# Kernel optimization log

Hardware: AMD Instinct MI355X
Metric: run time of the kernel (lower is better)

The kernel has to match this reference:

```python
import jax, jax.numpy as jnp
import numpy as np

NUM_HEADS = 8
D_MODEL = 512
HEAD_DIM = D_MODEL // NUM_HEADS
LN_EPS = 1e-5


def setup_inputs() -> dict:
    key = jax.random.key(0)
    ks = jax.random.split(key, 12)
    B, S = 8, 1024
    P = 2 * S - 1  # relative position length
    s = 0.02
    return {
        "x": jax.random.normal(ks[0], (B, S, D_MODEL), jnp.float32),
        "pos_emb": jax.random.normal(ks[1], (P, D_MODEL), jnp.float32),
        "ln_w": jnp.ones((D_MODEL,), jnp.float32),
        "ln_b": jnp.zeros((D_MODEL,), jnp.float32),
        "Wq": jax.random.normal(ks[2], (D_MODEL, D_MODEL), jnp.float32) * s,
        "bq": jax.random.normal(ks[3], (D_MODEL,), jnp.float32) * s,
        "Wk": jax.random.normal(ks[4], (D_MODEL, D_MODEL), jnp.float32) * s,
        "bk": jax.random.normal(ks[5], (D_MODEL,), jnp.float32) * s,
        "Wv": jax.random.normal(ks[6], (D_MODEL, D_MODEL), jnp.float32) * s,
        "bv": jax.random.normal(ks[7], (D_MODEL,), jnp.float32) * s,
        "Wo": jax.random.normal(ks[8], (D_MODEL, D_MODEL), jnp.float32) * s,
        "bo": jax.random.normal(ks[9], (D_MODEL,), jnp.float32) * s,
        "Wp": jax.random.normal(ks[10], (D_MODEL, D_MODEL), jnp.float32) * s,
        "pos_bias_u": jax.random.normal(ks[11], (D_MODEL,), jnp.float32) * s,
        "pos_bias_v": jax.random.normal(jax.random.fold_in(key, 99), (D_MODEL,), jnp.float32) * s,
    }


def _rel_shift(x):
    # x: [B, H, S, P] -> Transformer-XL relative shift, return [B, H, S, S]
    b, h, s, p = x.shape
    x = jnp.pad(x, ((0, 0), (0, 0), (0, 0), (1, 0)))  # pad one zero column on left
    x = x.reshape(b, h, p + 1, s)[:, :, 1:, :]
    x = x.reshape(b, h, s, p)
    return x[:, :, :, :s]


def reference(x, pos_emb, ln_w, ln_b, Wq, bq, Wk, bk, Wv, bv, Wo, bo, Wp,
              pos_bias_u, pos_bias_v):
    B, S, D = x.shape
    H, hd = NUM_HEADS, HEAD_DIM
    # LayerNorm
    mu = jnp.mean(x, axis=-1, keepdims=True)
    var = jnp.mean(jnp.square(x - mu), axis=-1, keepdims=True)
    h_ = (x - mu) * jax.lax.rsqrt(var + LN_EPS) * ln_w + ln_b
    # Projections (torch Linear: y = x @ W.T + b)
    q = (h_ @ Wq.T + bq).reshape(B, S, H, hd).transpose(0, 2, 1, 3)  # [B,H,S,hd]
    k = (h_ @ Wk.T + bk).reshape(B, S, H, hd).transpose(0, 2, 1, 3)
    v = (h_ @ Wv.T + bv).reshape(B, S, H, hd).transpose(0, 2, 1, 3)
    bias_u = pos_bias_u.reshape(1, H, 1, hd)
    bias_v = pos_bias_v.reshape(1, H, 1, hd)
    content = jnp.einsum('bhqd,bhkd->bhqk', q + bias_u, k)
    # Positional projection: [P, D] -> [H, P, hd]
    p = (pos_emb @ Wp.T).reshape(-1, H, hd).transpose(1, 0, 2)
    pos_score = jnp.einsum('bhqd,hpd->bhqp', q + bias_v, p)
    pos_score = _rel_shift(pos_score)
    scale = 1.0 / np.sqrt(hd).astype(np.float32)
    attn = jax.nn.softmax((content + pos_score) * scale, axis=-1)
    out = jnp.einsum('bhqk,bhkd->bhqd', attn, v)
    out = out.transpose(0, 2, 1, 3).reshape(B, S, D)
    out = out @ Wo.T + bo
    return x + out
```

## Files before the change

kernel.cpp:

```cpp
#include <hip/hip_runtime.h>
#include <hip/hip_bf16.h>


typedef __attribute__((ext_vector_type(8))) short  s16x8;
typedef __attribute__((ext_vector_type(4))) short  s16x4;
typedef __attribute__((ext_vector_type(8))) __bf16 bfv8;
typedef __attribute__((ext_vector_type(4))) float  f32x4;

__device__ __forceinline__ float b2f(short s){
  unsigned u = ((unsigned)(unsigned short)s) << 16;
  float f; __builtin_memcpy(&f, &u, 4); return f;
}
__device__ __forceinline__ short f2b(float f){
  unsigned u; __builtin_memcpy(&u, &f, 4);
  u = (u + 0x7fffu + ((u >> 16) & 1u)) >> 16;
  return (short)u;
}
__device__ __forceinline__ f32x4 MFMA(s16x8 a, s16x8 b, f32x4 c){
  return __builtin_amdgcn_mfma_f32_16x16x32_bf16(
      __builtin_bit_cast(bfv8, a), __builtin_bit_cast(bfv8, b), c, 0, 0, 0);
}
__device__ __forceinline__ void gload_lds16(const void* g, void* l){
  __builtin_amdgcn_global_load_lds(
      (const __attribute__((address_space(1))) void*)g,
      (__attribute__((address_space(3))) void*)l, 16, 0, 0);
}
__device__ __forceinline__ void cvt8(const float* in, short* out, size_t i8){
  f32x4 a = *(const f32x4*)(in + i8*8);
  f32x4 b = *(const f32x4*)(in + i8*8 + 4);
  short o[8];
  o[0]=f2b(a[0]); o[1]=f2b(a[1]); o[2]=f2b(a[2]); o[3]=f2b(a[3]);
  o[4]=f2b(b[0]); o[5]=f2b(b[1]); o[6]=f2b(b[2]); o[7]=f2b(b[3]);
  *(s16x8*)(out + i8*8) = *(s16x8*)o;
}

__global__ __launch_bounds__(256) void prep_kernel(
    const float* __restrict__ Wq, const float* __restrict__ Wk,
    const float* __restrict__ Wv, const float* __restrict__ Wo,
    const float* __restrict__ Wp, const float* __restrict__ pos,
    const float* __restrict__ x, const float* __restrict__ lnw, const float* __restrict__ lnb,
    short* __restrict__ wqkv, short* __restrict__ wo, short* __restrict__ wp,
    short* __restrict__ posbf, short* __restrict__ h_bf)
{
  int bid = blockIdx.x, tid = threadIdx.x;
  if(bid < 640){
    int w = bid >> 7;
    size_t i = (size_t)(bid & 127)*256 + tid;
    const float* src; short* dst;
    if(w == 0){ src = Wq; dst = wqkv; }
    else if(w == 1){ src = Wk; dst = wqkv + 262144; }
    else if(w == 2){ src = Wv; dst = wqkv + 524288; }
    else if(w == 3){ src = Wo; dst = wo; }
    else { src = Wp; dst = wp; }
    cvt8(src, dst, i);
  } else if(bid < 1152){
    size_t i = (size_t)(bid - 640)*256 + tid;
    if(i < 131008) cvt8(pos, posbf, i);
  } else {
    int row = (bid - 1152)*4 + (tid >> 6);
    int lane = tid & 63;
    const float* xr = x + (size_t)row*512;
    f32x4 v0 = *(const f32x4*)(xr + lane*8);
    f32x4 v1 = *(const f32x4*)(xr + lane*8 + 4);
    float s  = v0[0]+v0[1]+v0[2]+v0[3]+v1[0]+v1[1]+v1[2]+v1[3];
    float s2 = v0[0]*v0[0]+v0[1]*v0[1]+v0[2]*v0[2]+v0[3]*v0[3]
             + v1[0]*v1[0]+v1[1]*v1[1]+v1[2]*v1[2]+v1[3]*v1[3];
    #pragma unroll
    for(int m=1;m<64;m<<=1){ s += __shfl_xor(s,m); s2 += __shfl_xor(s2,m); }
    float mu = s * (1.0f/512.0f);
    float rs = rsqrtf(s2*(1.0f/512.0f) - mu*mu + 1e-5f);
    short o[8];
    #pragma unroll
    for(int e=0;e<8;e++){
      float xv = (e<4)? v0[e] : v1[e-4];
      int d = lane*8 + e;
      o[e] = f2b((xv - mu)*rs*lnw[d] + lnb[d]);
    }
    *(s16x8*)(h_bf + (size_t)row*512 + lane*8) = *(s16x8*)o;
  }
}

__global__ __launch_bounds__(256) void gemm_fused(
    const short* __restrict__ h_bf, const short* __restrict__ wqkv,
    const float* __restrict__ bq, const float* __restrict__ bk, const float* __restrict__ bv,
    const short* __restrict__ posbf, const short* __restrict__ wp,
    short* __restrict__ q_sw, short* __restrict__ k_sw, short* __restrict__ v_sw,
    short* __restrict__ p_sw)
{
  __shared__ __align__(16) short At[128*32];
  __shared__ __align__(16) short Bt[128*32];
  int bid = blockIdx.x, tid = threadIdx.x;
  int wave = tid >> 6, lane = tid & 63;
  int quad = lane >> 4, l16 = lane & 15;
  int srow = lane >> 2, scol = (lane & 3)*8;
  if(bid < 768){
    int bx = bid % 12, by = bid / 12;
    int m0 = by*128, n0 = bx*128;
    int wm = wave >> 1, wn = wave & 1;
    f32x4 acc[4][4] = {};
    for(int k0=0; k0<512; k0+=32){
      #pragma unroll
      for(int c=0;c<2;c++){
        int rb = (wave + 4*c)*16;
        gload_lds16(h_bf + (size_t)(m0 + rb + srow)*512 + k0 + scol, At + rb*32);
        gload_lds16(wqkv + (size_t)(n0 + rb + srow)*512 + k0 + scol, Bt + rb*32);
      }
      __syncthreads();
      s16x8 af[4], bfr[4];
      #pragma unroll
      for(int i=0;i<4;i++) af[i]  = *(const s16x8*)(At + (wm*64 + i*16 + l16)*32 + quad*8);
      #pragma unroll
      for(int j=0;j<4;j++) bfr[j] = *(const s16x8*)(Bt + (wn*64 + j*16 + l16)*32 + quad*8);
      #pragma unroll
      for(int i=0;i<4;i++)
        #pragma unroll
        for(int j=0;j<4;j++)
          acc[i][j] = MFMA(af[i], bfr[j], acc[i][j]);
      __syncthreads();
    }
    #pragma unroll
    for(int i=0;i<4;i++){
      int rowb = m0 + wm*64 + i*16 + quad*4;
      #pragma unroll
      for(int j=0;j<4;j++){
        int colg = n0 + wn*64 + j*16 + l16;
        int seg = colg >> 9, c = colg & 511;
        float bias = (seg == 0) ? bq[c] : (seg == 1) ? bk[c] : bv[c];
        int hh = c >> 6;
        if(seg < 2){
          int ks = (c>>5)&1, qd = (c>>3)&3, e = c&7;
          int tblk = (rowb>>4)&63, bb = rowb>>10;
          short* dst = seg ? k_sw : q_sw;
          size_t base = ((size_t)((((bb*8+hh)*64+tblk)*2+ks)*64) + qd*16)*8 + e;
          #pragma unroll
          for(int r=0;r<4;r++)
            dst[base + (size_t)(quad*4+r)*8] = f2b(acc[i][j][r] + bias);
        } else {
          int ds = (c>>4)&3, l16p = c&15;
          int jt = (rowb>>6)&15, jk = (rowb>>5)&1, qd = (rowb>>3)&3, e0 = rowb&7;
          int bb = rowb>>10;
          short o4[4];
          #pragma unroll
          for(int r=0;r<4;r++) o4[r] = f2b(acc[i][j][r] + bias);
          size_t base = ((size_t)(((((bb*8+hh)*16+jt)*4+ds)*2+jk)*64) + qd*16 + l16p)*8 + e0;
          *(s16x4*)(v_sw + base) = *(s16x4*)o4;
        }
      }
    }
  } else {
    int pid = bid - 768;
    int bx = pid % 8, by = pid / 8;
    int m0 = by*64, n0 = bx*64;
    int wm = wave >> 1, wn = wave & 1;
    f32x4 acc[2][2] = {};
    for(int k0=0; k0<512; k0+=32){
      int rb = wave*16;
      int ra = m0 + rb + srow; if(ra > 2046) ra = 2046;
      gload_lds16(posbf + (size_t)ra*512 + k0 + scol, At + rb*32);
      gload_lds16(wp + (size_t)(n0 + rb + srow)*512 + k0 + scol, Bt + rb*32);
      __syncthreads();
      s16x8 af[2], bfr[2];
      #pragma unroll
      for(int i=0;i<2;i++) af[i]  = *(const s16x8*)(At + (wm*32 + i*16 + l16)*32 + quad*8);
      #pragma unroll
      for(int j=0;j<2;j++) bfr[j] = *(const s16x8*)(Bt + (wn*32 + j*16 + l16)*32 + quad*8);
      #pragma unroll
      for(int i=0;i<2;i++)
        #pragma unroll
        for(int j=0;j<2;j++)
          acc[i][j] = MFMA(af[i], bfr[j], acc[i][j]);
      __syncthreads();
    }
    #pragma unroll
    for(int i=0;i<2;i++){
      int rowb = m0 + wm*32 + i*16 + quad*4;
      #pragma unroll
      for(int j=0;j<2;j++){
        int col = n0 + wn*32 + j*16 + l16;
        int hh = col>>6, ks = (col>>5)&1, qd = (col>>3)&3, e = col&7;
        int rblk = rowb>>4;
        size_t base = ((size_t)(((hh*128+rblk)*2+ks)*64) + qd*16)*8 + e;
        #pragma unroll
        for(int r=0;r<4;r++)
          p_sw[base + (size_t)(quad*4+r)*8] = f2b(acc[i][j][r]);
      }
    }
  }
}

__global__ __launch_bounds__(256) void attn_kernel(
    const short* __restrict__ q_sw, const short* __restrict__ k_sw,
    const short* __restrict__ v_sw, const short* __restrict__ p_sw,
    const float* __restrict__ bu, const float* __restrict__ bvv,
    short* __restrict__ out)
{
  __shared__ __align__(16) float combf[4160];
  int tid = threadIdx.x;
  int wave = tid >> 6, lane = tid & 63, quad = lane >> 4, l16 = lane & 15;
  int h = blockIdx.y, b = blockIdx.z, bh = b*8 + h;
  int iblk = blockIdx.x;
  int iw = iblk*16;
  short* pw = (short*)combf + wave*1152;

  const short* qb = q_sw + (size_t)bh*65536;
  const short* kb = k_sw + (size_t)bh*65536;
  const short* vb = v_sw + (size_t)bh*65536;
  const short* pb = p_sw + (size_t)h*131072;

  s16x8 qu[2], qv[2];
  #pragma unroll
  for(int ks=0;ks<2;ks++){
    s16x8 qr = *(const s16x8*)(qb + ((size_t)(iblk*2+ks)*64 + lane)*8);
    short tu[8], tv[8];
    #pragma unroll
    for(int e=0;e<8;e++){
      int d = h*64 + ks*32 + quad*8 + e;
      float f = b2f(qr[e]);
      tu[e] = f2b((f + bu[d]) * 0.125f);
      tv[e] = f2b((f + bvv[d]) * 0.125f);
    }
    qu[ks] = *(s16x8*)tu; qv[ks] = *(s16x8*)tv;
  }

  f32x4 oacc[4] = {};
  float lpart[4] = {0.f, 0.f, 0.f, 0.f};

  #pragma unroll
  for(int t=0; t<4; t++){
    int jt = wave*4 + t;
    f32x4 sc[4];
    #pragma unroll
    for(int js=0;js<4;js++){
      f32x4 a = {};
      #pragma unroll
      for(int ks=0;ks<2;ks++){
        s16x8 kf = *(const s16x8*)(kb + ((size_t)((jt*4+js)*2+ks)*64 + lane)*8);
        a = MFMA(qu[ks], kf, a);
      }
      sc[js] = a;
    }
    int rb0 = (jt*64 - iw + 1008) >> 4;
    f32x4 ps[5];
    #pragma unroll
    for(int nt=0;nt<5;nt++){
      f32x4 a = {};
      #pragma unroll
      for(int ks=0;ks<2;ks++){
        s16x8 pf = *(const s16x8*)(pb + ((size_t)((rb0+nt)*2+ks)*64 + lane)*8);
        a = MFMA(qv[ks], pf, a);
      }
      ps[nt] = a;
    }
    #pragma unroll
    for(int r=0;r<4;r++){
      int il = quad*4 + r;
      int srcl = quad*16 + ((l16 + 15 - il) & 15);
      float rot[5];
      #pragma unroll
      for(int nt=0;nt<5;nt++) rot[nt] = __shfl(ps[nt][r], srcl);
      bool lo = (l16 <= il);
      #pragma unroll
      for(int js=0;js<4;js++){
        float sv = sc[js][r] + (lo ? rot[js] : rot[js+1]);
        float pe = __expf(sv);
        lpart[r] += pe;
        pw[il*72 + js*16 + l16] = f2b(pe);
      }
    }
    #pragma unroll
    for(int jk=0;jk<2;jk++){
      s16x8 pf = *(const s16x8*)(pw + l16*72 + jk*32 + quad*8);
      #pragma unroll
      for(int ds=0;ds<4;ds++){
        s16x8 vf = *(const s16x8*)(vb + ((size_t)((jt*4+ds)*2+jk)*64 + lane)*8);
        oacc[ds] = MFMA(pf, vf, oacc[ds]);
      }
    }
  }
  #pragma unroll
  for(int r=0;r<4;r++){
    float l = lpart[r];
    #pragma unroll
    for(int m=1;m<16;m<<=1) l += __shfl_xor(l, m);
    lpart[r] = l;
  }
  __syncthreads();
  float* comb  = combf;
  float* lcomb = combf + 4096;
  #pragma unroll
  for(int e=0;e<16;e++) comb[wave*1024 + e*64 + lane] = oacc[e>>2][e&3];
  if(l16 == 0){
    #pragma unroll
    for(int r=0;r<4;r++) lcomb[wave*16 + quad*4 + r] = lpart[r];
  }
  __syncthreads();
  #pragma unroll
  for(int i=0;i<4;i++){
    int s = i*256 + tid;
    int e = s >> 6, lsrc = s & 63;
    int ds = e >> 2, rr = e & 3;
    int il = (lsrc >> 4)*4 + rr;
    int dim = ds*16 + (lsrc & 15);
    float o = comb[s] + comb[1024+s] + comb[2048+s] + comb[3072+s];
    float l = lcomb[il] + lcomb[16+il] + lcomb[32+il] + lcomb[48+il];
    out[((size_t)(b*1024 + iw + il)*512) + h*64 + dim] = f2b(o / l);
  }
}

__global__ __launch_bounds__(256) void gemm_out(
    const short* __restrict__ A, const short* __restrict__ B,
    const float* __restrict__ bias, const float* __restrict__ resid,
    float* __restrict__ Cout)
{
  __shared__ __align__(16) short At[64*32];
  __shared__ __align__(16) short Bt[64*32];
  int tid = threadIdx.x;
  int wave = tid >> 6, lane = tid & 63;
  int quad = lane >> 4, l16 = lane & 15;
  int wm = wave >> 1, wn = wave & 1;
  int m0 = blockIdx.y*64, n0 = blockIdx.x*64;
  int srow = lane >> 2, scol = (lane & 3)*8;
  f32x4 acc[2][2] = {};
  for(int k0=0; k0<512; k0+=32){
    int rb = wave*16;
    gload_lds16(A + (size_t)(m0 + rb + srow)*512 + k0 + scol, At + rb*32);
    gload_lds16(B + (size_t)(n0 + rb + srow)*512 + k0 + scol, Bt + rb*32);
    __syncthreads();
    s16x8 af[2], bfr[2];
    #pragma unroll
    for(int i=0;i<2;i++) af[i]  = *(const s16x8*)(At + (wm*32 + i*16 + l16)*32 + quad*8);
    #pragma unroll
    for(int j=0;j<2;j++) bfr[j] = *(const s16x8*)(Bt + (wn*32 + j*16 + l16)*32 + quad*8);
    #pragma unroll
    for(int i=0;i<2;i++)
      #pragma unroll
      for(int j=0;j<2;j++)
        acc[i][j] = MFMA(af[i], bfr[j], acc[i][j]);
    __syncthreads();
  }
  #pragma unroll
  for(int i=0;i<2;i++){
    int rowb = m0 + wm*32 + i*16 + quad*4;
    #pragma unroll
    for(int j=0;j<2;j++){
      int col = n0 + wn*32 + j*16 + l16;
      float bv = bias[col];
      #pragma unroll
      for(int r=0;r<4;r++){
        size_t idx = (size_t)(rowb + r)*512 + col;
        Cout[idx] = acc[i][j][r] + bv + resid[idx];
      }
    }
  }
}

extern "C" void kernel_launch(void* const* d_in, const int* in_sizes, int n_in,
                              void* d_out, int out_size, void* d_ws, size_t ws_size,
                              hipStream_t stream)
{
  const float* x    = (const float*)d_in[0];
  const float* pos  = (const float*)d_in[1];
  const float* lnw  = (const float*)d_in[2];
  const float* lnb  = (const float*)d_in[3];
  const float* Wq   = (const float*)d_in[4];
  const float* bq   = (const float*)d_in[5];
  const float* Wk   = (const float*)d_in[6];
  const float* bk   = (const float*)d_in[7];
  const float* Wv   = (const float*)d_in[8];
  const float* bv   = (const float*)d_in[9];
  const float* Wo   = (const float*)d_in[10];
  const float* bo   = (const float*)d_in[11];
  const float* Wp   = (const float*)d_in[12];
  const float* pbu  = (const float*)d_in[13];
  const float* pbv  = (const float*)d_in[14];
  float* out = (float*)d_out;

  char* ws = (char*)d_ws;
  short* h_bf    = (short*)(ws);
  short* q_sw    = (short*)(ws + ( 8u<<20));
  short* k_sw    = (short*)(ws + (16u<<20));
  short* v_sw    = (short*)(ws + (24u<<20));
  short* a_bf    = (short*)(ws + (32u<<20));
  short* p_sw    = (short*)(ws + (40u<<20));
  short* pos_bf  = (short*)(ws + (42u<<20));
  short* wqkv_bf = (short*)(ws + (44u<<20));
  short* wo_bf   = (short*)(ws + (47u<<20));
  short* wp_bf   = (short*)(ws + (47u<<20) + (512u<<10));

  prep_kernel<<<dim3(3200), 256, 0, stream>>>(Wq, Wk, Wv, Wo, Wp, pos,
                                              x, lnw, lnb,
                                              wqkv_bf, wo_bf, wp_bf, pos_bf, h_bf);
  gemm_fused<<<dim3(1024), 256, 0, stream>>>(h_bf, wqkv_bf, bq, bk, bv,
                                             pos_bf, wp_bf,
                                             q_sw, k_sw, v_sw, p_sw);
  attn_kernel<<<dim3(64,8,8), 256, 0, stream>>>(q_sw, k_sw, v_sw, p_sw, pbu, pbv, a_bf);
  gemm_out<<<dim3(8,128), 256, 0, stream>>>(a_bf, wo_bf, bo, x, out);
  (void)in_sizes; (void)n_in; (void)out_size; (void)ws_size;
}
```

Measured before the change: 233.3 us.

## Stage QKV epilogue through LDS, use packed bf16 converts and exp2 softmax

```diff
diff --git a/kernel.cpp b/kernel.cpp
--- a/kernel.cpp
+++ b/kernel.cpp
@@ -3,7 +3,6 @@
 
 
 typedef __attribute__((ext_vector_type(8))) short  s16x8;
-typedef __attribute__((ext_vector_type(4))) short  s16x4;
 typedef __attribute__((ext_vector_type(8))) __bf16 bfv8;
 typedef __attribute__((ext_vector_type(4))) float  f32x4;
 
@@ -16,6 +15,10 @@
   u = (u + 0x7fffu + ((u >> 16) & 1u)) >> 16;
   return (short)u;
 }
+__device__ __forceinline__ unsigned pk2(float lo, float hi){
+  __hip_bfloat162 t = __float22bfloat162_rn(make_float2(lo, hi));
+  unsigned u; __builtin_memcpy(&u, &t, 4); return u;
+}
 __device__ __forceinline__ f32x4 MFMA(s16x8 a, s16x8 b, f32x4 c){
   return __builtin_amdgcn_mfma_f32_16x16x32_bf16(
       __builtin_bit_cast(bfv8, a), __builtin_bit_cast(bfv8, b), c, 0, 0, 0);
@@ -25,13 +28,14 @@
       (const __attribute__((address_space(1))) void*)g,
       (__attribute__((address_space(3))) void*)l, 16, 0, 0);
 }
+typedef __attribute__((ext_vector_type(4))) unsigned u32x4;
 __device__ __forceinline__ void cvt8(const float* in, short* out, size_t i8){
   f32x4 a = *(const f32x4*)(in + i8*8);
   f32x4 b = *(const f32x4*)(in + i8*8 + 4);
-  short o[8];
-  o[0]=f2b(a[0]); o[1]=f2b(a[1]); o[2]=f2b(a[2]); o[3]=f2b(a[3]);
-  o[4]=f2b(b[0]); o[5]=f2b(b[1]); o[6]=f2b(b[2]); o[7]=f2b(b[3]);
-  *(s16x8*)(out + i8*8) = *(s16x8*)o;
+  u32x4 o;
+  o[0] = pk2(a[0],a[1]); o[1] = pk2(a[2],a[3]);
+  o[2] = pk2(b[0],b[1]); o[3] = pk2(b[2],b[3]);
+  *(u32x4*)(out + i8*8) = o;
 }
 
 __global__ __launch_bounds__(256) void prep_kernel(
@@ -69,14 +73,16 @@
     for(int m=1;m<64;m<<=1){ s += __shfl_xor(s,m); s2 += __shfl_xor(s2,m); }
     float mu = s * (1.0f/512.0f);
     float rs = rsqrtf(s2*(1.0f/512.0f) - mu*mu + 1e-5f);
-    short o[8];
+    float y[8];
     #pragma unroll
     for(int e=0;e<8;e++){
       float xv = (e<4)? v0[e] : v1[e-4];
       int d = lane*8 + e;
-      o[e] = f2b((xv - mu)*rs*lnw[d] + lnb[d]);
-    }
-    *(s16x8*)(h_bf + (size_t)row*512 + lane*8) = *(s16x8*)o;
+      y[e] = (xv - mu)*rs*lnw[d] + lnb[d];
+    }
+    u32x4 o;
+    o[0]=pk2(y[0],y[1]); o[1]=pk2(y[2],y[3]); o[2]=pk2(y[4],y[5]); o[3]=pk2(y[6],y[7]);
+    *(u32x4*)(h_bf + (size_t)row*512 + lane*8) = o;
   }
 }
 
@@ -87,8 +93,9 @@
     short* __restrict__ q_sw, short* __restrict__ k_sw, short* __restrict__ v_sw,
     short* __restrict__ p_sw)
 {
-  __shared__ __align__(16) short At[128*32];
-  __shared__ __align__(16) short Bt[128*32];
+  __shared__ __align__(16) short smem[9216];
+  short* At = smem;
+  short* Bt = smem + 4096;
   int bid = blockIdx.x, tid = threadIdx.x;
   int wave = tid >> 6, lane = tid & 63;
   int quad = lane >> 4, l16 = lane & 15;
@@ -118,33 +125,75 @@
           acc[i][j] = MFMA(af[i], bfr[j], acc[i][j]);
       __syncthreads();
     }
-    #pragma unroll
-    for(int i=0;i<4;i++){
-      int rowb = m0 + wm*64 + i*16 + quad*4;
-      #pragma unroll
-      for(int j=0;j<4;j++){
-        int colg = n0 + wn*64 + j*16 + l16;
-        int seg = colg >> 9, c = colg & 511;
-        float bias = (seg == 0) ? bq[c] : (seg == 1) ? bk[c] : bv[c];
-        int hh = c >> 6;
-        if(seg < 2){
-          int ks = (c>>5)&1, qd = (c>>3)&3, e = c&7;
-          int tblk = (rowb>>4)&63, bb = rowb>>10;
-          short* dst = seg ? k_sw : q_sw;
-          size_t base = ((size_t)((((bb*8+hh)*64+tblk)*2+ks)*64) + qd*16)*8 + e;
+    int seg = bx >> 2;
+    int nseg = (bx & 3)*128;
+    int bb = by >> 3;
+    const float* bsrc = (seg==0)? bq : (seg==1)? bk : bv;
+    float bias_j[4];
+    #pragma unroll
+    for(int j=0;j<4;j++) bias_j[j] = bsrc[nseg + wn*64 + j*16 + l16];
+    if(seg < 2){
+      short* dst = seg ? k_sw : q_sw;
+      #pragma unroll
+      for(int h2=0; h2<2; h2++){
+        if(wm == h2){
           #pragma unroll
-          for(int r=0;r<4;r++)
-            dst[base + (size_t)(quad*4+r)*8] = f2b(acc[i][j][r] + bias);
-        } else {
-          int ds = (c>>4)&3, l16p = c&15;
-          int jt = (rowb>>6)&15, jk = (rowb>>5)&1, qd = (rowb>>3)&3, e0 = rowb&7;
-          int bb = rowb>>10;
-          short o4[4];
+          for(int i=0;i<4;i++){
+            int lr = i*16 + quad*4;
+            #pragma unroll
+            for(int j=0;j<4;j++){
+              int cl = wn*64 + j*16 + l16;
+              unsigned p01 = pk2(acc[i][j][0]+bias_j[j], acc[i][j][1]+bias_j[j]);
+              unsigned p23 = pk2(acc[i][j][2]+bias_j[j], acc[i][j][3]+bias_j[j]);
+              smem[(lr+0)*136 + cl] = (short)p01;
+              smem[(lr+1)*136 + cl] = (short)(p01>>16);
+              smem[(lr+2)*136 + cl] = (short)p23;
+              smem[(lr+3)*136 + cl] = (short)(p23>>16);
+            }
+          }
+        }
+        __syncthreads();
+        #pragma unroll
+        for(int it=0; it<4; it++){
+          int ci = it*4 + wave;
+          int hs = ci >> 2, tb = ci & 3;
+          s16x8 vv = *(const s16x8*)(smem + (tb*16 + l16)*136 + hs*32 + quad*8);
+          int hh = (nseg>>6) + (hs>>1);
+          int tg = ((m0 + h2*64)>>4) + tb;
+          size_t chunk = ((size_t)((bb*8 + hh)*64 + tg))*2 + (hs&1);
+          *(s16x8*)(dst + chunk*512 + (size_t)lane*8) = vv;
+        }
+        __syncthreads();
+      }
+    } else {
+      #pragma unroll
+      for(int h2=0; h2<2; h2++){
+        int jt = by*2 + h2;
+        if(wm == h2){
           #pragma unroll
-          for(int r=0;r<4;r++) o4[r] = f2b(acc[i][j][r] + bias);
-          size_t base = ((size_t)(((((bb*8+hh)*16+jt)*4+ds)*2+jk)*64) + qd*16 + l16p)*8 + e0;
-          *(s16x4*)(v_sw + base) = *(s16x4*)o4;
+          for(int i=0;i<4;i++){
+            int tl = i*16 + quad*4;
+            #pragma unroll
+            for(int j=0;j<4;j++){
+              int dl = wn*64 + j*16 + l16;
+              unsigned p01 = pk2(acc[i][j][0]+bias_j[j], acc[i][j][1]+bias_j[j]);
+              unsigned p23 = pk2(acc[i][j][2]+bias_j[j], acc[i][j][3]+bias_j[j]);
+              unsigned* w2 = (unsigned*)(smem + dl*72 + tl);
+              w2[0] = p01; w2[1] = p23;
+            }
+          }
         }
+        __syncthreads();
+        #pragma unroll
+        for(int it=0; it<4; it++){
+          int ci = it*4 + wave;
+          int hl = ci>>3, ds = (ci>>1)&3, jk = ci&1;
+          s16x8 vv = *(const s16x8*)(smem + (hl*64 + ds*16 + l16)*72 + jk*32 + quad*8);
+          int hh = (nseg>>6) + hl;
+          size_t chunk = (((size_t)((bb*8 + hh)*16 + jt))*4 + ds)*2 + jk;
+          *(s16x8*)(v_sw + chunk*512 + (size_t)lane*8) = vv;
+        }
+        __syncthreads();
       }
     }
   } else {
@@ -207,6 +256,7 @@
   const short* vb = v_sw + (size_t)bh*65536;
   const short* pb = p_sw + (size_t)h*131072;
 
+  const float S2 = 0.125f * 1.44269504f;
   s16x8 qu[2], qv[2];
   #pragma unroll
   for(int ks=0;ks<2;ks++){
@@ -216,10 +266,18 @@
     for(int e=0;e<8;e++){
       int d = h*64 + ks*32 + quad*8 + e;
       float f = b2f(qr[e]);
-      tu[e] = f2b((f + bu[d]) * 0.125f);
-      tv[e] = f2b((f + bvv[d]) * 0.125f);
+      tu[e] = f2b((f + bu[d]) * S2);
+      tv[e] = f2b((f + bvv[d]) * S2);
     }
     qu[ks] = *(s16x8*)tu; qv[ks] = *(s16x8*)tv;
+  }
+
+  int srcl[4]; bool lo[4];
+  #pragma unroll
+  for(int r=0;r<4;r++){
+    int il = quad*4 + r;
+    srcl[r] = quad*16 + ((l16 + 15 - il) & 15);
+    lo[r]   = (l16 <= il);
   }
 
   f32x4 oacc[4] = {};
@@ -251,21 +309,29 @@
       }
       ps[nt] = a;
     }
+    float pe[4][4];
     #pragma unroll
     for(int r=0;r<4;r++){
-      int il = quad*4 + r;
-      int srcl = quad*16 + ((l16 + 15 - il) & 15);
       float rot[5];
       #pragma unroll
-      for(int nt=0;nt<5;nt++) rot[nt] = __shfl(ps[nt][r], srcl);
-      bool lo = (l16 <= il);
+      for(int nt=0;nt<5;nt++) rot[nt] = __shfl(ps[nt][r], srcl[r]);
       #pragma unroll
       for(int js=0;js<4;js++){
-        float sv = sc[js][r] + (lo ? rot[js] : rot[js+1]);
-        float pe = __expf(sv);
-        lpart[r] += pe;
-        pw[il*72 + js*16 + l16] = f2b(pe);
-      }
+        float sv = sc[js][r] + (lo[r] ? rot[js] : rot[js+1]);
+        float p = exp2f(sv);
+        pe[js][r] = p;
+        lpart[r] += p;
+      }
+    }
+    #pragma unroll
+    for(int js=0;js<4;js++){
+      int col = js*16 + l16;
+      unsigned p01 = pk2(pe[js][0], pe[js][1]);
+      unsigned p23 = pk2(pe[js][2], pe[js][3]);
+      pw[(quad*4+0)*72 + col] = (short)p01;
+      pw[(quad*4+1)*72 + col] = (short)(p01>>16);
+      pw[(quad*4+2)*72 + col] = (short)p23;
+      pw[(quad*4+3)*72 + col] = (short)(p23>>16);
     }
     #pragma unroll
     for(int jk=0;jk<2;jk++){
@@ -303,7 +369,8 @@
     int dim = ds*16 + (lsrc & 15);
     float o = comb[s] + comb[1024+s] + comb[2048+s] + comb[3072+s];
     float l = lcomb[il] + lcomb[16+il] + lcomb[32+il] + lcomb[48+il];
-    out[((size_t)(b*1024 + iw + il)*512) + h*64 + dim] = f2b(o / l);
+    float rl = __builtin_amdgcn_rcpf(l);
+    out[((size_t)(b*1024 + iw + il)*512) + h*64 + dim] = f2b(o * rl);
   }
 }
 
```

After: 222.1 us. -4.8%, faster.
